# Optimization experiments

Hardware: AMD Instinct MI355X
Metric: run time of the kernel (lower is better)

The kernel has to match this reference:

```python
import jax, jax.numpy as jnp
import numpy as np

N_NODES = 50000
N_EDGES = 1600000
N_FEAT, N_HID, N_CLASS = 256, 128, 64


def setup_inputs() -> dict:
    key = jax.random.key(0)
    ks = jax.random.split(key, 8)
    x = jax.random.normal(ks[0], (N_NODES, N_FEAT), dtype=jnp.float32)
    edge_index = jax.random.randint(ks[1], (2, N_EDGES), 0, N_NODES, dtype=jnp.int64)
    edge_weight = jax.random.uniform(ks[2], (N_EDGES,), dtype=jnp.float32)
    # Glorot-style init for GCNConv weights, zero bias (PyG defaults)
    W1 = jax.random.normal(ks[3], (N_FEAT, N_HID), dtype=jnp.float32) * (1.0 / np.sqrt(N_FEAT))
    b1 = jnp.zeros((N_HID,), dtype=jnp.float32)
    W2 = jax.random.normal(ks[4], (N_HID, N_CLASS), dtype=jnp.float32) * (1.0 / np.sqrt(N_HID))
    b2 = jnp.zeros((N_CLASS,), dtype=jnp.float32)
    return {"x": x, "edge_index": edge_index, "edge_weight": edge_weight,
            "W1": W1, "b1": b1, "W2": W2, "b2": b2}


def _gcn_norm(edge_index, edge_weight, num_nodes):
    # add self loops with weight 1 (GCNConv add_self_loops=True)
    loop = jnp.arange(num_nodes, dtype=edge_index.dtype)
    row = jnp.concatenate([edge_index[0], loop])
    col = jnp.concatenate([edge_index[1], loop])
    ew = jnp.concatenate([edge_weight, jnp.ones((num_nodes,), dtype=edge_weight.dtype)])
    # symmetric normalization: deg computed on target (col) nodes
    deg = jax.ops.segment_sum(ew, col, num_segments=num_nodes)
    dinv = jnp.where(deg > 0, jax.lax.rsqrt(deg), 0.0)
    norm = dinv[row] * ew * dinv[col]
    return row, col, norm


def _gcn_conv(h, row, col, norm, W, b, num_nodes):
    h = h @ W                       # [N, out]
    msgs = h[row] * norm[:, None]   # [E+N, out] gather + scale
    out = jax.ops.segment_sum(msgs, col, num_segments=num_nodes)  # scatter-add to targets
    return out + b


def reference(x, edge_index, edge_weight, W1, b1, W2, b2):
    n = x.shape[0]
    row, col, norm = _gcn_norm(edge_index, edge_weight, n)
    h = jax.nn.sigmoid(_gcn_conv(x, row, col, norm, W1, b1, n))
    out = jnp.tanh(_gcn_conv(h, row, col, norm, W2, b2, n))
    return out
```

## Files before the change

### kernel.cpp

```cpp
#include <hip/hip_runtime.h>
#include <math.h>

#define N_NODES 50000
#define N_EDGES 1600000
#define N_FEAT  256
#define N_HID   128
#define N_CLASS 64
#define SCAN_NBLK ((N_NODES + 1023) / 1024)
#define FIXSCALE 268435456.0f

typedef __attribute__((ext_vector_type(8))) short short8v;
typedef __attribute__((ext_vector_type(4))) float float4v;

__device__ __forceinline__ unsigned int f2bf(float f) {
  unsigned int u = __float_as_uint(f);
  unsigned int r = (u + 0x7fffu + ((u >> 16) & 1u)) >> 16;
  return r & 0xffffu;
}

__global__ __launch_bounds__(256) void transpose_w_kernel(
    const float* __restrict__ W, unsigned short* __restrict__ WT, int K, int N) {
  int i = blockIdx.x * 256 + threadIdx.x;
  if (i >= N * K) return;
  int n = i / K, k = i % K;
  WT[i] = (unsigned short)f2bf(W[(size_t)k * N + n]);
}

__global__ __launch_bounds__(256) void deg_rank_kernel(
    const int* __restrict__ col, const float* __restrict__ ew,
    unsigned long long* __restrict__ packed, unsigned short* __restrict__ rank, int E) {
  int e = blockIdx.x * 256 + threadIdx.x;
  if (e >= E) return;
  int c = col[e];
  unsigned long long fix = (unsigned long long)__float2uint_rn(ew[e] * FIXSCALE);
  unsigned long long old = atomicAdd(&packed[c], (1ULL << 40) | fix);
  rank[e] = (unsigned short)(old >> 40);
}

__global__ __launch_bounds__(256) void scan1_kernel(
    const unsigned long long* __restrict__ packed, int* __restrict__ rowptr,
    int* __restrict__ partials, float* __restrict__ dinv) {
  __shared__ int wsum[4];
  __shared__ int woff[4];
  int t = threadIdx.x, b = blockIdx.x;
  int base = b * 1024 + t * 4;
  int v0 = 0, v1 = 0, v2 = 0, v3 = 0;
#pragma unroll
  for (int j = 0; j < 4; ++j) {
    int i = base + j;
    if (i < N_NODES) {
      unsigned long long p = packed[i];
      int c = (int)(p >> 40);
      float deg = (float)(long long)(p & 0xFFFFFFFFFFULL) * (1.0f / FIXSCALE);
      dinv[i] = rsqrtf(deg + 1.0f);
      if (j == 0) v0 = c; else if (j == 1) v1 = c; else if (j == 2) v2 = c; else v3 = c;
    }
  }
  int s1 = v0 + v1, s2 = s1 + v2, s3 = s2 + v3;
  int lane = t & 63, w = t >> 6;
  int inc = s3;
#pragma unroll
  for (int off = 1; off < 64; off <<= 1) {
    int u = __shfl_up(inc, off, 64);
    if (lane >= off) inc += u;
  }
  if (lane == 63) wsum[w] = inc;
  __syncthreads();
  if (t == 0) {
    int a = 0;
#pragma unroll
    for (int i = 0; i < 4; ++i) { woff[i] = a; a += wsum[i]; }
    partials[b] = a;
  }
  __syncthreads();
  int ex = woff[w] + inc - s3;
  if (base + 0 < N_NODES) rowptr[base + 0] = ex;
  if (base + 1 < N_NODES) rowptr[base + 1] = ex + v0;
  if (base + 2 < N_NODES) rowptr[base + 2] = ex + s1;
  if (base + 3 < N_NODES) rowptr[base + 3] = ex + s2;
}

__global__ void scan2_kernel(int* __restrict__ partials, int* __restrict__ rowptr) {
  if (threadIdx.x == 0 && blockIdx.x == 0) {
    int a = 0;
    for (int i = 0; i < SCAN_NBLK; ++i) { int x = partials[i]; partials[i] = a; a += x; }
    rowptr[N_NODES] = a;
  }
}

__global__ __launch_bounds__(256) void scan3_kernel(
    int* __restrict__ rowptr, const int* __restrict__ partials) {
  int i = blockIdx.x * 256 + threadIdx.x;
  if (i < N_NODES) rowptr[i] += partials[i >> 10];
}

__global__ __launch_bounds__(256) void scatter_kernel(
    const int* __restrict__ row, const int* __restrict__ col,
    const float* __restrict__ ew, const unsigned short* __restrict__ rank,
    const float* __restrict__ dinv, const int* __restrict__ rowptr,
    int2* __restrict__ ep, int E) {
  int e = blockIdx.x * 256 + threadIdx.x;
  if (e >= E) return;
  int r = row[e], c = col[e];
  float w = dinv[r] * ew[e] * dinv[c];
  int pos = rowptr[c] + (int)rank[e];
  ep[pos] = make_int2(r, __float_as_int(w));
}

template <int BN, int K, bool AFP32>
__global__ __launch_bounds__(256) void mfma_gemm_kernel(
    const void* __restrict__ Ain, const unsigned short* __restrict__ BT,
    unsigned short* __restrict__ C, int M) {
  constexpr int BM = 64, BK = 64;
  constexpr int NT = BN / 16;
  __shared__ unsigned char AsB[BM * 128];
  __shared__ unsigned char BsB[BN * 128];
  int t = threadIdx.x;
  int lane = t & 63, wv = t >> 6;
  int m0 = blockIdx.x * BM;

  float4v acc[NT];
#pragma unroll
  for (int i = 0; i < NT; ++i) acc[i] = (float4v){0.f, 0.f, 0.f, 0.f};

  for (int k0 = 0; k0 < K; k0 += BK) {
    {
      int r = t >> 2, q = t & 3;
      int gr = m0 + r;
      unsigned int swz = (unsigned int)((r & 7) << 4);
      uint4 o0 = make_uint4(0, 0, 0, 0), o1 = make_uint4(0, 0, 0, 0);
      if constexpr (AFP32) {
        const float* A = (const float*)Ain;
        if (gr < M) {
          const float* p = &A[(size_t)gr * K + k0 + q * 16];
          float4 v0 = *(const float4*)(p + 0), v1 = *(const float4*)(p + 4);
          float4 v2 = *(const float4*)(p + 8), v3 = *(const float4*)(p + 12);
          o0.x = f2bf(v0.x) | (f2bf(v0.y) << 16); o0.y = f2bf(v0.z) | (f2bf(v0.w) << 16);
          o0.z = f2bf(v1.x) | (f2bf(v1.y) << 16); o0.w = f2bf(v1.z) | (f2bf(v1.w) << 16);
          o1.x = f2bf(v2.x) | (f2bf(v2.y) << 16); o1.y = f2bf(v2.z) | (f2bf(v2.w) << 16);
          o1.z = f2bf(v3.x) | (f2bf(v3.y) << 16); o1.w = f2bf(v3.z) | (f2bf(v3.w) << 16);
        }
      } else {
        const unsigned short* A = (const unsigned short*)Ain;
        if (gr < M) {
          const unsigned short* p = &A[(size_t)gr * K + k0 + q * 16];
          o0 = *(const uint4*)(p);
          o1 = *(const uint4*)(p + 8);
        }
      }
      *(uint4*)(AsB + r * 128 + (((unsigned)(q * 32)) ^ swz)) = o0;
      *(uint4*)(AsB + r * 128 + (((unsigned)(q * 32 + 16)) ^ swz)) = o1;
    }
    {
      constexpr int BPT = BN / 2;
      constexpr int TPR = 128 / BPT;
      int br = t / TPR;
      int bo = (t % TPR) * BPT;
      unsigned int swz = (unsigned int)((br & 7) << 4);
#pragma unroll
      for (int s = 0; s < BPT / 16; ++s) {
        uint4 v = *(const uint4*)&BT[(size_t)br * K + k0 + (bo + s * 16) / 2];
        *(uint4*)(BsB + br * 128 + (((unsigned)(bo + s * 16)) ^ swz)) = v;
      }
    }
    __syncthreads();
    {
      int ar = wv * 16 + (lane & 15);
      int g = lane >> 4;
      unsigned int aswz = (unsigned int)((ar & 7) << 4);
      unsigned int bswz = (unsigned int)((lane & 7) << 4);
#pragma unroll
      for (int kk = 0; kk < BK; kk += 32) {
        short8v af = *(const short8v*)(AsB + ar * 128 +
                                       (((unsigned)(kk * 2 + g * 16)) ^ aswz));
#pragma unroll
        for (int nt = 0; nt < NT; ++nt) {
          int brr = nt * 16 + (lane & 15);
          short8v bf = *(const short8v*)(BsB + brr * 128 +
                                         (((unsigned)(kk * 2 + g * 16)) ^ bswz));
          acc[nt] = __builtin_amdgcn_mfma_f32_16x16x32_bf16(af, bf, acc[nt], 0, 0, 0);
        }
      }
    }
    __syncthreads();
  }
  int r0 = m0 + wv * 16 + (lane >> 4) * 4;
  int c0 = lane & 15;
#pragma unroll
  for (int nt = 0; nt < NT; ++nt) {
#pragma unroll
    for (int j = 0; j < 4; ++j) {
      int gr = r0 + j;
      if (gr < M) C[(size_t)gr * BN + nt * 16 + c0] = (unsigned short)f2bf(acc[nt][j]);
    }
  }
}

__global__ __launch_bounds__(256) void agg128_kernel(
    const unsigned short* __restrict__ h, const int* __restrict__ rowptr,
    const int2* __restrict__ ep, const float* __restrict__ dinv,
    const float* __restrict__ bias, unsigned short* __restrict__ out, int n) {
  int wid  = (int)((blockIdx.x * 256 + threadIdx.x) >> 6);
  int lane = threadIdx.x & 63;
  if (wid >= n) return;
  int s = rowptr[wid], e_end = rowptr[wid + 1];
  unsigned int f2 = 2u * lane;
  float a0 = 0.f, a1 = 0.f, b0 = 0.f, b1 = 0.f,
        c0 = 0.f, c1 = 0.f, d0 = 0.f, d1 = 0.f;
  int e = s;
  for (; e + 3 < e_end; e += 4) {
    int2 p0 = ep[e], p1 = ep[e + 1], p2 = ep[e + 2], p3 = ep[e + 3];
    unsigned int h0 = *(const unsigned int*)(h + ((size_t)p0.x << 7) + f2);
    unsigned int h1 = *(const unsigned int*)(h + ((size_t)p1.x << 7) + f2);
    unsigned int h2 = *(const unsigned int*)(h + ((size_t)p2.x << 7) + f2);
    unsigned int h3 = *(const unsigned int*)(h + ((size_t)p3.x << 7) + f2);
    float w0 = __int_as_float(p0.y), w1 = __int_as_float(p1.y);
    float w2 = __int_as_float(p2.y), w3 = __int_as_float(p3.y);
    a0 = fmaf(w0, __uint_as_float(h0 << 16), a0);
    a1 = fmaf(w0, __uint_as_float(h0 & 0xffff0000u), a1);
    b0 = fmaf(w1, __uint_as_float(h1 << 16), b0);
    b1 = fmaf(w1, __uint_as_float(h1 & 0xffff0000u), b1);
    c0 = fmaf(w2, __uint_as_float(h2 << 16), c0);
    c1 = fmaf(w2, __uint_as_float(h2 & 0xffff0000u), c1);
    d0 = fmaf(w3, __uint_as_float(h3 << 16), d0);
    d1 = fmaf(w3, __uint_as_float(h3 & 0xffff0000u), d1);
  }
  for (; e < e_end; ++e) {
    int2 p0 = ep[e];
    unsigned int h0 = *(const unsigned int*)(h + ((size_t)p0.x << 7) + f2);
    float w0 = __int_as_float(p0.y);
    a0 = fmaf(w0, __uint_as_float(h0 << 16), a0);
    a1 = fmaf(w0, __uint_as_float(h0 & 0xffff0000u), a1);
  }
  float di = dinv[wid], sw = di * di;
  unsigned int hs = *(const unsigned int*)(h + ((size_t)wid << 7) + f2);
  a0 = fmaf(sw, __uint_as_float(hs << 16), a0);
  a1 = fmaf(sw, __uint_as_float(hs & 0xffff0000u), a1);
  float v0 = (a0 + b0) + (c0 + d0) + bias[f2];
  float v1 = (a1 + b1) + (c1 + d1) + bias[f2 + 1];
  v0 = 1.f / (1.f + expf(-v0));
  v1 = 1.f / (1.f + expf(-v1));
  unsigned int o = f2bf(v0) | (f2bf(v1) << 16);
  *(unsigned int*)(out + ((size_t)wid << 7) + f2) = o;
}

__global__ __launch_bounds__(256) void agg64_kernel(
    const unsigned short* __restrict__ h, const int* __restrict__ rowptr,
    const int2* __restrict__ ep, const float* __restrict__ dinv,
    const float* __restrict__ bias, float* __restrict__ out, int n) {
  int wid  = (int)((blockIdx.x * 256 + threadIdx.x) >> 6);
  int lane = threadIdx.x & 63;
  if (wid >= n) return;
  int half = lane >> 5, ll = lane & 31;
  unsigned int f2 = 2u * ll;
  int s = rowptr[wid], e_end = rowptr[wid + 1];
  float a0 = 0.f, a1 = 0.f, b0 = 0.f, b1 = 0.f,
        c0 = 0.f, c1 = 0.f, d0 = 0.f, d1 = 0.f;
  int e = s + half;
  for (; e + 6 < e_end; e += 8) {
    int2 p0 = ep[e], p1 = ep[e + 2], p2 = ep[e + 4], p3 = ep[e + 6];
    unsigned int h0 = *(const unsigned int*)(h + ((size_t)p0.x << 6) + f2);
    unsigned int h1 = *(const unsigned int*)(h + ((size_t)p1.x << 6) + f2);
    unsigned int h2 = *(const unsigned int*)(h + ((size_t)p2.x << 6) + f2);
    unsigned int h3 = *(const unsigned int*)(h + ((size_t)p3.x << 6) + f2);
    float w0 = __int_as_float(p0.y), w1 = __int_as_float(p1.y);
    float w2 = __int_as_float(p2.y), w3 = __int_as_float(p3.y);
    a0 = fmaf(w0, __uint_as_float(h0 << 16), a0);
    a1 = fmaf(w0, __uint_as_float(h0 & 0xffff0000u), a1);
    b0 = fmaf(w1, __uint_as_float(h1 << 16), b0);
    b1 = fmaf(w1, __uint_as_float(h1 & 0xffff0000u), b1);
    c0 = fmaf(w2, __uint_as_float(h2 << 16), c0);
    c1 = fmaf(w2, __uint_as_float(h2 & 0xffff0000u), c1);
    d0 = fmaf(w3, __uint_as_float(h3 << 16), d0);
    d1 = fmaf(w3, __uint_as_float(h3 & 0xffff0000u), d1);
  }
  for (; e < e_end; e += 2) {
    int2 p0 = ep[e];
    unsigned int h0 = *(const unsigned int*)(h + ((size_t)p0.x << 6) + f2);
    float w0 = __int_as_float(p0.y);
    a0 = fmaf(w0, __uint_as_float(h0 << 16), a0);
    a1 = fmaf(w0, __uint_as_float(h0 & 0xffff0000u), a1);
  }
  a0 = (a0 + b0) + (c0 + d0);
  a1 = (a1 + b1) + (c1 + d1);
  if (half == 0) {
    float di = dinv[wid], sw = di * di;
    unsigned int hs = *(const unsigned int*)(h + ((size_t)wid << 6) + f2);
    a0 = fmaf(sw, __uint_as_float(hs << 16), a0);
    a1 = fmaf(sw, __uint_as_float(hs & 0xffff0000u), a1);
  }
  a0 += __shfl_xor(a0, 32, 64);
  a1 += __shfl_xor(a1, 32, 64);
  if (half == 0) {
    float v0 = tanhf(a0 + bias[f2]);
    float v1 = tanhf(a1 + bias[f2 + 1]);
    *(float2*)&out[(size_t)wid * 64 + f2] = make_float2(v0, v1);
  }
}

extern "C" void kernel_launch(void* const* d_in, const int* in_sizes, int n_in,
                              void* d_out, int out_size, void* d_ws, size_t ws_size,
                              hipStream_t stream) {
  const float* x  = (const float*)d_in[0];
  const int*   ei = (const int*)d_in[1];
  const float* ew = (const float*)d_in[2];
  const float* W1 = (const float*)d_in[3];
  const float* b1 = (const float*)d_in[4];
  const float* W2 = (const float*)d_in[5];
  const float* b2 = (const float*)d_in[6];
  float* out = (float*)d_out;

  const int* row = ei;
  const int* col = ei + N_EDGES;

  char* ws = (char*)d_ws;
  size_t off = 0;
  auto alloc = [&](size_t bytes) {
    void* p = ws + off;
    off = (off + bytes + 255) & ~(size_t)255;
    return p;
  };
  unsigned long long* packed = (unsigned long long*)alloc(N_NODES * 8);
  int*   rowptr   = (int*)alloc((N_NODES + 1) * 4);
  float* dinv     = (float*)alloc(N_NODES * 4);
  int*   partials = (int*)alloc(SCAN_NBLK * 4);
  unsigned short* rank = (unsigned short*)alloc((size_t)N_EDGES * 2);
  int2*  ep       = (int2*)alloc((size_t)N_EDGES * 8);
  unsigned short* W1T  = (unsigned short*)alloc((size_t)N_HID * N_FEAT * 2);
  unsigned short* W2T  = (unsigned short*)alloc((size_t)N_CLASS * N_HID * 2);
  unsigned short* bufA = (unsigned short*)alloc((size_t)N_NODES * N_HID * 2);
  unsigned short* bufB = (unsigned short*)alloc((size_t)N_NODES * N_HID * 2);
  unsigned short* bufC = (unsigned short*)alloc((size_t)N_NODES * N_CLASS * 2);

  hipMemsetAsync(packed, 0, N_NODES * 8, stream);

  int eblocks = (N_EDGES + 255) / 256;
  int nblocks = (N_NODES + 255) / 256;
  int gblocks = (N_NODES + 63) / 64;

  transpose_w_kernel<<<(N_HID * N_FEAT + 255) / 256, 256, 0, stream>>>(W1, W1T, N_FEAT, N_HID);
  transpose_w_kernel<<<(N_CLASS * N_HID + 255) / 256, 256, 0, stream>>>(W2, W2T, N_HID, N_CLASS);

  deg_rank_kernel<<<eblocks, 256, 0, stream>>>(col, ew, packed, rank, N_EDGES);
  scan1_kernel<<<SCAN_NBLK, 256, 0, stream>>>(packed, rowptr, partials, dinv);
  scan2_kernel<<<1, 64, 0, stream>>>(partials, rowptr);
  scan3_kernel<<<nblocks, 256, 0, stream>>>(rowptr, partials);
  scatter_kernel<<<eblocks, 256, 0, stream>>>(row, col, ew, rank, dinv, rowptr, ep, N_EDGES);

  mfma_gemm_kernel<N_HID, N_FEAT, true><<<gblocks, 256, 0, stream>>>(x, W1T, bufA, N_NODES);
  agg128_kernel<<<(N_NODES * 64 + 255) / 256, 256, 0, stream>>>(
      bufA, rowptr, ep, dinv, b1, bufB, N_NODES);

  mfma_gemm_kernel<N_CLASS, N_HID, false><<<gblocks, 256, 0, stream>>>(bufB, W2T, bufC, N_NODES);
  agg64_kernel<<<(N_NODES * 64 + 255) / 256, 256, 0, stream>>>(
      bufC, rowptr, ep, dinv, b2, out, N_NODES);
}
```

Before: 350.0 us.

## Pack edge payload to 32 bits and fuse degree pass with first GEMM

Each CSR edge entry shrinks from an int2 (int index plus fp32 weight) to one 32-bit word holding a 16-bit source index and an fp16 normalized weight. This halves edge-list traffic in scatter and in both aggregation kernels. The weight transpose kernels are removed: the GEMM now reads the fp32 W directly and converts it to bf16 while staging into shared memory. The degree/rank atomic pass and the first GEMM share one launch via block-index partitioning, so the two can overlap. The packing depends on node ids fitting in 16 bits and gives up some weight precision by storing it as fp16.

```diff
diff --git a/kernel.cpp b/kernel.cpp
--- a/kernel.cpp
+++ b/kernel.cpp
@@ -1,4 +1,5 @@
 #include <hip/hip_runtime.h>
+#include <hip/hip_fp16.h>
 #include <math.h>
 
 #define N_NODES 50000
@@ -8,6 +9,8 @@
 #define N_CLASS 64
 #define SCAN_NBLK ((N_NODES + 1023) / 1024)
 #define FIXSCALE 268435456.0f
+#define EBLK ((N_EDGES + 255) / 256)
+#define GBLK ((N_NODES + 63) / 64)
 
 typedef __attribute__((ext_vector_type(8))) short short8v;
 typedef __attribute__((ext_vector_type(4))) float float4v;
@@ -18,106 +21,16 @@
   return r & 0xffffu;
 }
 
-__global__ __launch_bounds__(256) void transpose_w_kernel(
-    const float* __restrict__ W, unsigned short* __restrict__ WT, int K, int N) {
-  int i = blockIdx.x * 256 + threadIdx.x;
-  if (i >= N * K) return;
-  int n = i / K, k = i % K;
-  WT[i] = (unsigned short)f2bf(W[(size_t)k * N + n]);
-}
-
-__global__ __launch_bounds__(256) void deg_rank_kernel(
-    const int* __restrict__ col, const float* __restrict__ ew,
-    unsigned long long* __restrict__ packed, unsigned short* __restrict__ rank, int E) {
-  int e = blockIdx.x * 256 + threadIdx.x;
-  if (e >= E) return;
-  int c = col[e];
-  unsigned long long fix = (unsigned long long)__float2uint_rn(ew[e] * FIXSCALE);
-  unsigned long long old = atomicAdd(&packed[c], (1ULL << 40) | fix);
-  rank[e] = (unsigned short)(old >> 40);
-}
-
-__global__ __launch_bounds__(256) void scan1_kernel(
-    const unsigned long long* __restrict__ packed, int* __restrict__ rowptr,
-    int* __restrict__ partials, float* __restrict__ dinv) {
-  __shared__ int wsum[4];
-  __shared__ int woff[4];
-  int t = threadIdx.x, b = blockIdx.x;
-  int base = b * 1024 + t * 4;
-  int v0 = 0, v1 = 0, v2 = 0, v3 = 0;
-#pragma unroll
-  for (int j = 0; j < 4; ++j) {
-    int i = base + j;
-    if (i < N_NODES) {
-      unsigned long long p = packed[i];
-      int c = (int)(p >> 40);
-      float deg = (float)(long long)(p & 0xFFFFFFFFFFULL) * (1.0f / FIXSCALE);
-      dinv[i] = rsqrtf(deg + 1.0f);
-      if (j == 0) v0 = c; else if (j == 1) v1 = c; else if (j == 2) v2 = c; else v3 = c;
-    }
-  }
-  int s1 = v0 + v1, s2 = s1 + v2, s3 = s2 + v3;
-  int lane = t & 63, w = t >> 6;
-  int inc = s3;
-#pragma unroll
-  for (int off = 1; off < 64; off <<= 1) {
-    int u = __shfl_up(inc, off, 64);
-    if (lane >= off) inc += u;
-  }
-  if (lane == 63) wsum[w] = inc;
-  __syncthreads();
-  if (t == 0) {
-    int a = 0;
-#pragma unroll
-    for (int i = 0; i < 4; ++i) { woff[i] = a; a += wsum[i]; }
-    partials[b] = a;
-  }
-  __syncthreads();
-  int ex = woff[w] + inc - s3;
-  if (base + 0 < N_NODES) rowptr[base + 0] = ex;
-  if (base + 1 < N_NODES) rowptr[base + 1] = ex + v0;
-  if (base + 2 < N_NODES) rowptr[base + 2] = ex + s1;
-  if (base + 3 < N_NODES) rowptr[base + 3] = ex + s2;
-}
-
-__global__ void scan2_kernel(int* __restrict__ partials, int* __restrict__ rowptr) {
-  if (threadIdx.x == 0 && blockIdx.x == 0) {
-    int a = 0;
-    for (int i = 0; i < SCAN_NBLK; ++i) { int x = partials[i]; partials[i] = a; a += x; }
-    rowptr[N_NODES] = a;
-  }
-}
-
-__global__ __launch_bounds__(256) void scan3_kernel(
-    int* __restrict__ rowptr, const int* __restrict__ partials) {
-  int i = blockIdx.x * 256 + threadIdx.x;
-  if (i < N_NODES) rowptr[i] += partials[i >> 10];
-}
-
-__global__ __launch_bounds__(256) void scatter_kernel(
-    const int* __restrict__ row, const int* __restrict__ col,
-    const float* __restrict__ ew, const unsigned short* __restrict__ rank,
-    const float* __restrict__ dinv, const int* __restrict__ rowptr,
-    int2* __restrict__ ep, int E) {
-  int e = blockIdx.x * 256 + threadIdx.x;
-  if (e >= E) return;
-  int r = row[e], c = col[e];
-  float w = dinv[r] * ew[e] * dinv[c];
-  int pos = rowptr[c] + (int)rank[e];
-  ep[pos] = make_int2(r, __float_as_int(w));
-}
-
 template <int BN, int K, bool AFP32>
-__global__ __launch_bounds__(256) void mfma_gemm_kernel(
-    const void* __restrict__ Ain, const unsigned short* __restrict__ BT,
-    unsigned short* __restrict__ C, int M) {
+__device__ __forceinline__ void gemm_body(
+    const void* __restrict__ Ain, const float* __restrict__ W,
+    unsigned short* __restrict__ C, int M, int m0) {
   constexpr int BM = 64, BK = 64;
   constexpr int NT = BN / 16;
   __shared__ unsigned char AsB[BM * 128];
   __shared__ unsigned char BsB[BN * 128];
   int t = threadIdx.x;
   int lane = t & 63, wv = t >> 6;
-  int m0 = blockIdx.x * BM;
 
   float4v acc[NT];
 #pragma unroll
@@ -152,15 +65,23 @@
       *(uint4*)(AsB + r * 128 + (((unsigned)(q * 32 + 16)) ^ swz)) = o1;
     }
     {
-      constexpr int BPT = BN / 2;
-      constexpr int TPR = 128 / BPT;
-      int br = t / TPR;
-      int bo = (t % TPR) * BPT;
-      unsigned int swz = (unsigned int)((br & 7) << 4);
-#pragma unroll
-      for (int s = 0; s < BPT / 16; ++s) {
-        uint4 v = *(const uint4*)&BT[(size_t)br * K + k0 + (bo + s * 16) / 2];
-        *(uint4*)(BsB + br * 128 + (((unsigned)(bo + s * 16)) ^ swz)) = v;
+      constexpr int N4 = BN / 4;
+      constexpr int KPP = 2 * (256 / N4);
+      int kp = t / N4, n4 = t % N4;
+#pragma unroll
+      for (int p = 0; p < BK / KPP; ++p) {
+        int k = p * KPP + kp * 2;
+        float4 va = *(const float4*)&W[(size_t)(k0 + k) * BN + n4 * 4];
+        float4 vb = *(const float4*)&W[(size_t)(k0 + k + 1) * BN + n4 * 4];
+        float fa[4] = {va.x, va.y, va.z, va.w};
+        float fb[4] = {vb.x, vb.y, vb.z, vb.w};
+#pragma unroll
+        for (int j = 0; j < 4; ++j) {
+          int n = n4 * 4 + j;
+          unsigned int val = f2bf(fa[j]) | (f2bf(fb[j]) << 16);
+          *(unsigned int*)(BsB + n * 128 +
+                           (((unsigned)(k * 2)) ^ ((unsigned)((n & 7) << 4)))) = val;
+        }
       }
     }
     __syncthreads();
@@ -196,9 +117,105 @@
   }
 }
 
+__global__ __launch_bounds__(256) void fusedA_kernel(
+    const float* __restrict__ x, const float* __restrict__ W1,
+    unsigned short* __restrict__ bufA,
+    const int* __restrict__ col, const float* __restrict__ ew,
+    unsigned long long* __restrict__ packed, unsigned short* __restrict__ rank) {
+  if (blockIdx.x < EBLK) {
+    int e = blockIdx.x * 256 + threadIdx.x;
+    if (e < N_EDGES) {
+      int c = col[e];
+      unsigned long long fix = (unsigned long long)__float2uint_rn(ew[e] * FIXSCALE);
+      unsigned long long old = atomicAdd(&packed[c], (1ULL << 40) | fix);
+      rank[e] = (unsigned short)(old >> 40);
+    }
+    return;
+  }
+  int m0 = (int)(blockIdx.x - EBLK) * 64;
+  gemm_body<N_HID, N_FEAT, true>(x, W1, bufA, N_NODES, m0);
+}
+
+__global__ __launch_bounds__(256) void gemm2_kernel(
+    const unsigned short* __restrict__ bufB, const float* __restrict__ W2,
+    unsigned short* __restrict__ bufC) {
+  gemm_body<N_CLASS, N_HID, false>(bufB, W2, bufC, N_NODES, (int)blockIdx.x * 64);
+}
+
+__global__ __launch_bounds__(256) void scan1_kernel(
+    const unsigned long long* __restrict__ packed, int* __restrict__ rowptr,
+    int* __restrict__ partials, float* __restrict__ dinv) {
+  __shared__ int wsum[4];
+  __shared__ int woff[4];
+  int t = threadIdx.x, b = blockIdx.x;
+  int base = b * 1024 + t * 4;
+  int v0 = 0, v1 = 0, v2 = 0, v3 = 0;
+#pragma unroll
+  for (int j = 0; j < 4; ++j) {
+    int i = base + j;
+    if (i < N_NODES) {
+      unsigned long long p = packed[i];
+      int c = (int)(p >> 40);
+      float deg = (float)(long long)(p & 0xFFFFFFFFFFULL) * (1.0f / FIXSCALE);
+      dinv[i] = rsqrtf(deg + 1.0f);
+      if (j == 0) v0 = c; else if (j == 1) v1 = c; else if (j == 2) v2 = c; else v3 = c;
+    }
+  }
+  int s1 = v0 + v1, s2 = s1 + v2, s3 = s2 + v3;
+  int lane = t & 63, w = t >> 6;
+  int inc = s3;
+#pragma unroll
+  for (int off = 1; off < 64; off <<= 1) {
+    int u = __shfl_up(inc, off, 64);
+    if (lane >= off) inc += u;
+  }
+  if (lane == 63) wsum[w] = inc;
+  __syncthreads();
+  if (t == 0) {
+    int a = 0;
+#pragma unroll
+    for (int i = 0; i < 4; ++i) { woff[i] = a; a += wsum[i]; }
+    partials[b] = a;
+  }
+  __syncthreads();
+  int ex = woff[w] + inc - s3;
+  if (base + 0 < N_NODES) rowptr[base + 0] = ex;
+  if (base + 1 < N_NODES) rowptr[base + 1] = ex + v0;
+  if (base + 2 < N_NODES) rowptr[base + 2] = ex + s1;
+  if (base + 3 < N_NODES) rowptr[base + 3] = ex + s2;
+}
+
+__global__ void scan2_kernel(int* __restrict__ partials, int* __restrict__ rowptr) {
+  if (threadIdx.x == 0 && blockIdx.x == 0) {
+    int a = 0;
+    for (int i = 0; i < SCAN_NBLK; ++i) { int x = partials[i]; partials[i] = a; a += x; }
+    rowptr[N_NODES] = a;
+  }
+}
+
+__global__ __launch_bounds__(256) void scan3_kernel(
+    int* __restrict__ rowptr, const int* __restrict__ partials) {
+  int i = blockIdx.x * 256 + threadIdx.x;
+  if (i < N_NODES) rowptr[i] += partials[i >> 10];
+}
+
+__global__ __launch_bounds__(256) void scatter_kernel(
+    const int* __restrict__ row, const int* __restrict__ col,
+    const float* __restrict__ ew, const unsigned short* __restrict__ rank,
+    const float* __restrict__ dinv, const int* __restrict__ rowptr,
+    unsigned int* __restrict__ ep, int E) {
+  int e = blockIdx.x * 256 + threadIdx.x;
+  if (e >= E) return;
+  int r = row[e], c = col[e];
+  float w = dinv[r] * ew[e] * dinv[c];
+  int pos = rowptr[c] + (int)rank[e];
+  unsigned int wh = (unsigned int)__half_as_ushort(__float2half(w));
+  ep[pos] = (unsigned int)r | (wh << 16);
+}
+
 __global__ __launch_bounds__(256) void agg128_kernel(
     const unsigned short* __restrict__ h, const int* __restrict__ rowptr,
-    const int2* __restrict__ ep, const float* __restrict__ dinv,
+    const unsigned int* __restrict__ ep, const float* __restrict__ dinv,
     const float* __restrict__ bias, unsigned short* __restrict__ out, int n) {
   int wid  = (int)((blockIdx.x * 256 + threadIdx.x) >> 6);
   int lane = threadIdx.x & 63;
@@ -209,13 +226,15 @@
         c0 = 0.f, c1 = 0.f, d0 = 0.f, d1 = 0.f;
   int e = s;
   for (; e + 3 < e_end; e += 4) {
-    int2 p0 = ep[e], p1 = ep[e + 1], p2 = ep[e + 2], p3 = ep[e + 3];
-    unsigned int h0 = *(const unsigned int*)(h + ((size_t)p0.x << 7) + f2);
-    unsigned int h1 = *(const unsigned int*)(h + ((size_t)p1.x << 7) + f2);
-    unsigned int h2 = *(const unsigned int*)(h + ((size_t)p2.x << 7) + f2);
-    unsigned int h3 = *(const unsigned int*)(h + ((size_t)p3.x << 7) + f2);
-    float w0 = __int_as_float(p0.y), w1 = __int_as_float(p1.y);
-    float w2 = __int_as_float(p2.y), w3 = __int_as_float(p3.y);
+    unsigned int p0 = ep[e], p1 = ep[e + 1], p2 = ep[e + 2], p3 = ep[e + 3];
+    unsigned int h0 = *(const unsigned int*)(h + ((size_t)(p0 & 0xffffu) << 7) + f2);
+    unsigned int h1 = *(const unsigned int*)(h + ((size_t)(p1 & 0xffffu) << 7) + f2);
+    unsigned int h2 = *(const unsigned int*)(h + ((size_t)(p2 & 0xffffu) << 7) + f2);
+    unsigned int h3 = *(const unsigned int*)(h + ((size_t)(p3 & 0xffffu) << 7) + f2);
+    float w0 = __half2float(__ushort_as_half((unsigned short)(p0 >> 16)));
+    float w1 = __half2float(__ushort_as_half((unsigned short)(p1 >> 16)));
+    float w2 = __half2float(__ushort_as_half((unsigned short)(p2 >> 16)));
+    float w3 = __half2float(__ushort_as_half((unsigned short)(p3 >> 16)));
     a0 = fmaf(w0, __uint_as_float(h0 << 16), a0);
     a1 = fmaf(w0, __uint_as_float(h0 & 0xffff0000u), a1);
     b0 = fmaf(w1, __uint_as_float(h1 << 16), b0);
@@ -226,9 +245,9 @@
     d1 = fmaf(w3, __uint_as_float(h3 & 0xffff0000u), d1);
   }
   for (; e < e_end; ++e) {
-    int2 p0 = ep[e];
-    unsigned int h0 = *(const unsigned int*)(h + ((size_t)p0.x << 7) + f2);
-    float w0 = __int_as_float(p0.y);
+    unsigned int p0 = ep[e];
+    unsigned int h0 = *(const unsigned int*)(h + ((size_t)(p0 & 0xffffu) << 7) + f2);
+    float w0 = __half2float(__ushort_as_half((unsigned short)(p0 >> 16)));
     a0 = fmaf(w0, __uint_as_float(h0 << 16), a0);
     a1 = fmaf(w0, __uint_as_float(h0 & 0xffff0000u), a1);
   }
@@ -246,7 +265,7 @@
 
 __global__ __launch_bounds__(256) void agg64_kernel(
     const unsigned short* __restrict__ h, const int* __restrict__ rowptr,
-    const int2* __restrict__ ep, const float* __restrict__ dinv,
+    const unsigned int* __restrict__ ep, const float* __restrict__ dinv,
     const float* __restrict__ bias, float* __restrict__ out, int n) {
   int wid  = (int)((blockIdx.x * 256 + threadIdx.x) >> 6);
   int lane = threadIdx.x & 63;
@@ -258,13 +277,15 @@
         c0 = 0.f, c1 = 0.f, d0 = 0.f, d1 = 0.f;
   int e = s + half;
   for (; e + 6 < e_end; e += 8) {
-    int2 p0 = ep[e], p1 = ep[e + 2], p2 = ep[e + 4], p3 = ep[e + 6];
-    unsigned int h0 = *(const unsigned int*)(h + ((size_t)p0.x << 6) + f2);
-    unsigned int h1 = *(const unsigned int*)(h + ((size_t)p1.x << 6) + f2);
-    unsigned int h2 = *(const unsigned int*)(h + ((size_t)p2.x << 6) + f2);
-    unsigned int h3 = *(const unsigned int*)(h + ((size_t)p3.x << 6) + f2);
-    float w0 = __int_as_float(p0.y), w1 = __int_as_float(p1.y);
-    float w2 = __int_as_float(p2.y), w3 = __int_as_float(p3.y);
+    unsigned int p0 = ep[e], p1 = ep[e + 2], p2 = ep[e + 4], p3 = ep[e + 6];
+    unsigned int h0 = *(const unsigned int*)(h + ((size_t)(p0 & 0xffffu) << 6) + f2);
+    unsigned int h1 = *(const unsigned int*)(h + ((size_t)(p1 & 0xffffu) << 6) + f2);
+    unsigned int h2 = *(const unsigned int*)(h + ((size_t)(p2 & 0xffffu) << 6) + f2);
+    unsigned int h3 = *(const unsigned int*)(h + ((size_t)(p3 & 0xffffu) << 6) + f2);
+    float w0 = __half2float(__ushort_as_half((unsigned short)(p0 >> 16)));
+    float w1 = __half2float(__ushort_as_half((unsigned short)(p1 >> 16)));
+    float w2 = __half2float(__ushort_as_half((unsigned short)(p2 >> 16)));
+    float w3 = __half2float(__ushort_as_half((unsigned short)(p3 >> 16)));
     a0 = fmaf(w0, __uint_as_float(h0 << 16), a0);
     a1 = fmaf(w0, __uint_as_float(h0 & 0xffff0000u), a1);
     b0 = fmaf(w1, __uint_as_float(h1 << 16), b0);
@@ -275,9 +296,9 @@
     d1 = fmaf(w3, __uint_as_float(h3 & 0xffff0000u), d1);
   }
   for (; e < e_end; e += 2) {
-    int2 p0 = ep[e];
-    unsigned int h0 = *(const unsigned int*)(h + ((size_t)p0.x << 6) + f2);
-    float w0 = __int_as_float(p0.y);
+    unsigned int p0 = ep[e];
+    unsigned int h0 = *(const unsigned int*)(h + ((size_t)(p0 & 0xffffu) << 6) + f2);
+    float w0 = __half2float(__ushort_as_half((unsigned short)(p0 >> 16)));
     a0 = fmaf(w0, __uint_as_float(h0 << 16), a0);
     a1 = fmaf(w0, __uint_as_float(h0 & 0xffff0000u), a1);
   }
@@ -325,33 +346,27 @@
   float* dinv     = (float*)alloc(N_NODES * 4);
   int*   partials = (int*)alloc(SCAN_NBLK * 4);
   unsigned short* rank = (unsigned short*)alloc((size_t)N_EDGES * 2);
-  int2*  ep       = (int2*)alloc((size_t)N_EDGES * 8);
-  unsigned short* W1T  = (unsigned short*)alloc((size_t)N_HID * N_FEAT * 2);
-  unsigned short* W2T  = (unsigned short*)alloc((size_t)N_CLASS * N_HID * 2);
+  unsigned int* ep = (unsigned int*)alloc((size_t)N_EDGES * 4);
   unsigned short* bufA = (unsigned short*)alloc((size_t)N_NODES * N_HID * 2);
   unsigned short* bufB = (unsigned short*)alloc((size_t)N_NODES * N_HID * 2);
   unsigned short* bufC = (unsigned short*)alloc((size_t)N_NODES * N_CLASS * 2);
 
   hipMemsetAsync(packed, 0, N_NODES * 8, stream);
 
-  int eblocks = (N_EDGES + 255) / 256;
+  int eblocks = EBLK;
   int nblocks = (N_NODES + 255) / 256;
-  int gblocks = (N_NODES + 63) / 64;
-
-  transpose_w_kernel<<<(N_HID * N_FEAT + 255) / 256, 256, 0, stream>>>(W1, W1T, N_FEAT, N_HID);
-  transpose_w_kernel<<<(N_CLASS * N_HID + 255) / 256, 256, 0, stream>>>(W2, W2T, N_HID, N_CLASS);
-
-  deg_rank_kernel<<<eblocks, 256, 0, stream>>>(col, ew, packed, rank, N_EDGES);
+
+  fusedA_kernel<<<EBLK + GBLK, 256, 0, stream>>>(x, W1, bufA, col, ew, packed, rank);
+
   scan1_kernel<<<SCAN_NBLK, 256, 0, stream>>>(packed, rowptr, partials, dinv);
   scan2_kernel<<<1, 64, 0, stream>>>(partials, rowptr);
   scan3_kernel<<<nblocks, 256, 0, stream>>>(rowptr, partials);
   scatter_kernel<<<eblocks, 256, 0, stream>>>(row, col, ew, rank, dinv, rowptr, ep, N_EDGES);
 
-  mfma_gemm_kernel<N_HID, N_FEAT, true><<<gblocks, 256, 0, stream>>>(x, W1T, bufA, N_NODES);
   agg128_kernel<<<(N_NODES * 64 + 255) / 256, 256, 0, stream>>>(
       bufA, rowptr, ep, dinv, b1, bufB, N_NODES);
 
-  mfma_gemm_kernel<N_CLASS, N_HID, false><<<gblocks, 256, 0, stream>>>(bufB, W2T, bufC, N_NODES);
+  gemm2_kernel<<<GBLK, 256, 0, stream>>>(bufB, W2, bufC);
   agg64_kernel<<<(N_NODES * 64 + 255) / 256, 256, 0, stream>>>(
       bufC, rowptr, ep, dinv, b2, out, N_NODES);
 }
```

After: 345.3 us. About the same (-1.4%).
